# Optimization experiments

Measured on AMD Instinct MI355X. Metric: run time of the kernel, lower is better.

Reference implementation:

```python
import jax, jax.numpy as jnp
import numpy as np

FILTERS = 256
KH, KW = 3, 3
SH, SW = 1, 1
IN_CH = 128


def setup_inputs() -> dict:
    key = jax.random.key(0)
    k1, k2 = jax.random.split(key)
    inputs = jax.random.normal(k1, (32, 112, 112, IN_CH), dtype=jnp.float32)
    # Glorot-uniform init matching the layer's build()
    limit = np.sqrt(6.0 / (KH * KW * IN_CH + FILTERS)).astype(np.float32)
    kernel = jax.random.uniform(k2, (KH, KW, IN_CH, FILTERS), dtype=jnp.float32,
                                minval=-limit, maxval=limit)
    bias = jnp.zeros((FILTERS,), dtype=jnp.float32)
    return {"inputs": inputs, "kernel": kernel, "bias": bias}


def reference(inputs, kernel, bias):
    # Equivalent math to extract_patches(SAME) + flattened matmul + bias:
    # a standard 2D convolution in NHWC with HWIO kernel.
    out = jax.lax.conv_general_dilated(
        inputs, kernel,
        window_strides=(SH, SW),
        padding="SAME",
        dimension_numbers=("NHWC", "HWIO", "NHWC"),
    )
    return out + bias
```

## Files before the change

### kernel.cpp

```cpp
#include <hip/hip_runtime.h>

typedef __attribute__((ext_vector_type(4))) float   floatx4;
typedef __attribute__((ext_vector_type(8))) __bf16  bf16x8;
typedef unsigned short ushort_t;
typedef __attribute__((ext_vector_type(8))) ushort_t ushortx8;

typedef const unsigned int __attribute__((address_space(1)))* gptr_t;
typedef unsigned int __attribute__((address_space(3)))* lptr_t;

#define NIMG 32
#define H    112
#define W    112
#define CIN  128
#define COUT 256
#define HP   114
#define WP   114

#define BM 128
#define BN 128
#define BK 32
#define KSTEPS 36

__device__ __forceinline__ ushort_t f32_to_bf16(float f) {
    unsigned u = __float_as_uint(f);
    unsigned r = 0x7fffu + ((u >> 16) & 1u);
    return (ushort_t)((u + r) >> 16);
}

__global__ __launch_bounds__(256) void prepad_input(const float* __restrict__ in,
                                                    ushort_t* __restrict__ pad) {
    int t   = blockIdx.x * 256 + threadIdx.x;
    int ic8 = t & 15;
    int sp  = t >> 4;
    int iw  = sp % WP;
    int sp2 = sp / WP;
    int ih  = sp2 % HP;
    int n   = sp2 / HP;
    ushortx8 v;
    if (ih >= 1 && ih <= H && iw >= 1 && iw <= W) {
        const float* src = in + ((size_t)((n * H + (ih - 1)) * W + (iw - 1))) * CIN + ic8 * 8;
        floatx4 a = *reinterpret_cast<const floatx4*>(src);
        floatx4 b = *reinterpret_cast<const floatx4*>(src + 4);
#pragma unroll
        for (int j = 0; j < 4; ++j) { v[j] = f32_to_bf16(a[j]); v[4 + j] = f32_to_bf16(b[j]); }
    } else {
#pragma unroll
        for (int j = 0; j < 8; ++j) v[j] = 0;
    }
    reinterpret_cast<ushortx8*>(pad)[t] = v;
}

__global__ __launch_bounds__(256) void wtrans(const float* __restrict__ k,
                                              ushort_t* __restrict__ wt) {
    int t    = blockIdx.x * 256 + threadIdx.x;
    int ic   = t & 127;
    int oc   = (t >> 7) & 255;
    int khkw = t >> 15;
    wt[t] = f32_to_bf16(k[((size_t)(khkw * CIN + ic)) * COUT + oc]);
}

__global__ __launch_bounds__(256) void conv_mfma(const ushort_t* __restrict__ pad,
                                                 const ushort_t* __restrict__ wt,
                                                 const float* __restrict__ bias,
                                                 float* __restrict__ out) {
    __shared__ __align__(16) ushort_t As[BM * BK];
    __shared__ __align__(16) ushort_t Bs[BN * BK];

    const int tid  = threadIdx.x;
    const int wid  = tid >> 6;
    const int lane = tid & 63;
    const int bm   = blockIdx.x >> 1;
    const int bn   = blockIdx.x & 1;

    const int rbase = wid * 32 + (lane >> 2);
    const int kc    = (lane & 3) * 8;

    const ushort_t* aptr[2];
#pragma unroll
    for (int i = 0; i < 2; ++i) {
        int m  = bm * BM + rbase + i * 16;
        int n  = m / (H * W);
        int r  = m % (H * W);
        int oh = r / W;
        int ow = r % W;
        aptr[i] = pad + ((size_t)((n * HP + oh) * WP + ow)) * CIN + kc;
    }
    const ushort_t* bptr[2];
#pragma unroll
    for (int i = 0; i < 2; ++i) {
        int ocr = bn * BN + rbase + i * 16;
        bptr[i] = wt + (size_t)ocr * CIN + kc;
    }
    ushort_t* asd[2];
    ushort_t* bsd[2];
#pragma unroll
    for (int i = 0; i < 2; ++i) {
        asd[i] = As + (wid * 2 + i) * 512;
        bsd[i] = Bs + (wid * 2 + i) * 512;
    }

    const int wr   = wid >> 1, wc = wid & 1;
    const int aoff = (wr * 64 + (lane & 15)) * BK + (lane >> 4) * 8;
    const int boff = (wc * 64 + (lane & 15)) * BK + (lane >> 4) * 8;

    floatx4 acc[4][4];
#pragma unroll
    for (int i = 0; i < 4; ++i)
#pragma unroll
        for (int j = 0; j < 4; ++j) acc[i][j] = (floatx4)0.0f;

    for (int kt = 0; kt < KSTEPS; ++kt) {
        const int kh   = kt / 12;
        const int kw   = (kt >> 2) % 3;
        const int ic0  = (kt & 3) * 32;
        const int offA = (kh * WP + kw) * CIN + ic0;
        const int offB = (kh * 3 + kw) * COUT * CIN + ic0;
#pragma unroll
        for (int i = 0; i < 2; ++i) {
            __builtin_amdgcn_global_load_lds((gptr_t)(aptr[i] + offA), (lptr_t)(asd[i]), 16, 0, 0);
            __builtin_amdgcn_global_load_lds((gptr_t)(bptr[i] + offB), (lptr_t)(bsd[i]), 16, 0, 0);
        }
        __syncthreads();

        bf16x8 af[4], bfr[4];
#pragma unroll
        for (int mi = 0; mi < 4; ++mi)
            af[mi] = *reinterpret_cast<const bf16x8*>(As + aoff + mi * 16 * BK);
#pragma unroll
        for (int ni = 0; ni < 4; ++ni)
            bfr[ni] = *reinterpret_cast<const bf16x8*>(Bs + boff + ni * 16 * BK);
#pragma unroll
        for (int mi = 0; mi < 4; ++mi)
#pragma unroll
            for (int ni = 0; ni < 4; ++ni)
                acc[mi][ni] = __builtin_amdgcn_mfma_f32_16x16x32_bf16(af[mi], bfr[ni], acc[mi][ni], 0, 0, 0);
        __syncthreads();
    }

    const int col0 = bn * BN + wc * 64 + (lane & 15);
    const int row0 = bm * BM + wr * 64 + (lane >> 4) * 4;
#pragma unroll
    for (int ni = 0; ni < 4; ++ni) {
        const float bv = bias[col0 + ni * 16];
#pragma unroll
        for (int mi = 0; mi < 4; ++mi) {
#pragma unroll
            for (int r = 0; r < 4; ++r) {
                out[(size_t)(row0 + mi * 16 + r) * COUT + (col0 + ni * 16)] = acc[mi][ni][r] + bv;
            }
        }
    }
}

extern "C" void kernel_launch(void* const* d_in, const int* in_sizes, int n_in,
                              void* d_out, int out_size, void* d_ws, size_t ws_size,
                              hipStream_t stream) {
    const float* input = (const float*)d_in[0];
    const float* kern  = (const float*)d_in[1];
    const float* bias  = (const float*)d_in[2];
    float* out         = (float*)d_out;

    ushort_t* pad = (ushort_t*)d_ws;
    ushort_t* wt  = pad + (size_t)NIMG * HP * WP * CIN;

    prepad_input<<<25992, 256, 0, stream>>>(input, pad);
    wtrans<<<1152, 256, 0, stream>>>(kern, wt);
    conv_mfma<<<6272, 256, 0, stream>>>(pad, wt, bias, out);
}
```

Baseline: 422.9 us.

## Rewrite implicit-GEMM conv kernel with 256x256 tiles, double-buffered swizzled LDS

Replaces the 128x128x32 single-buffered conv kernel with a 512-thread, 256x256x64 tile kernel that covers all output channels per block. Loads go into double-buffered LDS with an XOR swizzle and are interleaved with MFMA phases, using explicit vmcnt waits, setprio and a block-index remap for L2 locality. The aim is more data reuse per loaded byte, fewer barriers per K step, and overlap of global loads with MFMA work. In exchange it uses 128KB of LDS and many accumulator registers, and the hand-written waitcnt and barrier sequencing is fragile.

Result: faster. 363.8 us (-14.0%).

```diff
diff --git a/kernel.cpp b/kernel.cpp
--- a/kernel.cpp
+++ b/kernel.cpp
@@ -15,11 +15,12 @@
 #define COUT 256
 #define HP   114
 #define WP   114
-
-#define BM 128
-#define BN 128
-#define BK 32
-#define KSTEPS 36
+#define HW   12544
+
+#define BM 256
+#define BN 256
+#define BK 64
+#define NT 18
 
 __device__ __forceinline__ ushort_t f32_to_bf16(float f) {
     unsigned u = __float_as_uint(f);
@@ -59,97 +60,130 @@
     wt[t] = f32_to_bf16(k[((size_t)(khkw * CIN + ic)) * COUT + oc]);
 }
 
-__global__ __launch_bounds__(256) void conv_mfma(const ushort_t* __restrict__ pad,
-                                                 const ushort_t* __restrict__ wt,
-                                                 const float* __restrict__ bias,
-                                                 float* __restrict__ out) {
-    __shared__ __align__(16) ushort_t As[BM * BK];
-    __shared__ __align__(16) ushort_t Bs[BN * BK];
+
+__device__ __forceinline__ int aoffK(int t) {
+    int tap = t >> 1;
+    return ((tap / 3) * WP + (tap % 3)) * CIN + (t & 1) * 64;
+}
+__device__ __forceinline__ int boffK(int t) {
+    int tap = t >> 1;
+    return tap * (COUT * CIN) + (t & 1) * 64;
+}
+
+__global__ __launch_bounds__(512, 2) void conv_mfma8(const ushort_t* __restrict__ pad,
+                                                     const ushort_t* __restrict__ wt,
+                                                     const float* __restrict__ bias,
+                                                     float* __restrict__ out) {
+    __shared__ __align__(16) ushort_t lds[65536];
 
     const int tid  = threadIdx.x;
     const int wid  = tid >> 6;
     const int lane = tid & 63;
-    const int bm   = blockIdx.x >> 1;
-    const int bn   = blockIdx.x & 1;
-
-    const int rbase = wid * 32 + (lane >> 2);
-    const int kc    = (lane & 3) * 8;
-
-    const ushort_t* aptr[2];
-#pragma unroll
-    for (int i = 0; i < 2; ++i) {
-        int m  = bm * BM + rbase + i * 16;
-        int n  = m / (H * W);
-        int r  = m % (H * W);
+    const int wm   = wid >> 2;
+    const int wn   = wid & 3;
+    const int bid  = blockIdx.x;
+    const int bm   = (bid & 7) * 196 + (bid >> 3);
+
+    const int trow = tid >> 3;
+    const int lc   = (tid & 7) ^ (trow & 7);
+
+    const ushort_t* srcA[4];
+    const ushort_t* srcB[4];
+#pragma unroll
+    for (int i = 0; i < 4; ++i) {
+        int m  = bm * BM + i * 64 + trow;
+        int n  = m / HW;
+        int r  = m % HW;
         int oh = r / W;
         int ow = r % W;
-        aptr[i] = pad + ((size_t)((n * HP + oh) * WP + ow)) * CIN + kc;
+        srcA[i] = pad + ((size_t)((n * HP + oh) * WP + ow)) * CIN + lc * 8;
+        int oc = i * 64 + trow;
+        srcB[i] = wt + (size_t)oc * CIN + lc * 8;
     }
-    const ushort_t* bptr[2];
-#pragma unroll
-    for (int i = 0; i < 2; ++i) {
-        int ocr = bn * BN + rbase + i * 16;
-        bptr[i] = wt + (size_t)ocr * CIN + kc;
-    }
-    ushort_t* asd[2];
-    ushort_t* bsd[2];
-#pragma unroll
-    for (int i = 0; i < 2; ++i) {
-        asd[i] = As + (wid * 2 + i) * 512;
-        bsd[i] = Bs + (wid * 2 + i) * 512;
-    }
-
-    const int wr   = wid >> 1, wc = wid & 1;
-    const int aoff = (wr * 64 + (lane & 15)) * BK + (lane >> 4) * 8;
-    const int boff = (wc * 64 + (lane & 15)) * BK + (lane >> 4) * 8;
-
-    floatx4 acc[4][4];
-#pragma unroll
-    for (int i = 0; i < 4; ++i)
+    const int dstSlot = wid * 512;
+
+#define STAGE_A(tile, half)                                                                         \
+    { int _o = aoffK(tile); int _b = ((tile) & 1) * 32768 + (half) * 8192 + dstSlot;                \
+      __builtin_amdgcn_global_load_lds((gptr_t)(srcA[(half)*2+0] + _o), (lptr_t)&lds[_b       ], 16, 0, 0); \
+      __builtin_amdgcn_global_load_lds((gptr_t)(srcA[(half)*2+1] + _o), (lptr_t)&lds[_b + 4096], 16, 0, 0); }
+#define STAGE_B(tile, half)                                                                         \
+    { int _o = boffK(tile); int _b = ((tile) & 1) * 32768 + 16384 + (half) * 8192 + dstSlot;        \
+      __builtin_amdgcn_global_load_lds((gptr_t)(srcB[(half)*2+0] + _o), (lptr_t)&lds[_b       ], 16, 0, 0); \
+      __builtin_amdgcn_global_load_lds((gptr_t)(srcB[(half)*2+1] + _o), (lptr_t)&lds[_b + 4096], 16, 0, 0); }
+
+    const int aBase = wm * 8192 + (lane & 15) * 64;
+    const int bBase = 16384 + (wn >> 1) * 8192 + ((wn & 1) * 64 + (lane & 15)) * 64;
+    int cOff[2];
+#pragma unroll
+    for (int ks = 0; ks < 2; ++ks)
+        cOff[ks] = ((ks * 4 + (lane >> 4)) ^ (lane & 7)) * 8;
+
+    floatx4 acc[8][4];
+#pragma unroll
+    for (int i = 0; i < 8; ++i)
 #pragma unroll
         for (int j = 0; j < 4; ++j) acc[i][j] = (floatx4)0.0f;
 
-    for (int kt = 0; kt < KSTEPS; ++kt) {
-        const int kh   = kt / 12;
-        const int kw   = (kt >> 2) % 3;
-        const int ic0  = (kt & 3) * 32;
-        const int offA = (kh * WP + kw) * CIN + ic0;
-        const int offB = (kh * 3 + kw) * COUT * CIN + ic0;
-#pragma unroll
-        for (int i = 0; i < 2; ++i) {
-            __builtin_amdgcn_global_load_lds((gptr_t)(aptr[i] + offA), (lptr_t)(asd[i]), 16, 0, 0);
-            __builtin_amdgcn_global_load_lds((gptr_t)(bptr[i] + offB), (lptr_t)(bsd[i]), 16, 0, 0);
-        }
-        __syncthreads();
-
-        bf16x8 af[4], bfr[4];
-#pragma unroll
-        for (int mi = 0; mi < 4; ++mi)
-            af[mi] = *reinterpret_cast<const bf16x8*>(As + aoff + mi * 16 * BK);
-#pragma unroll
-        for (int ni = 0; ni < 4; ++ni)
-            bfr[ni] = *reinterpret_cast<const bf16x8*>(Bs + boff + ni * 16 * BK);
-#pragma unroll
-        for (int mi = 0; mi < 4; ++mi)
-#pragma unroll
-            for (int ni = 0; ni < 4; ++ni)
-                acc[mi][ni] = __builtin_amdgcn_mfma_f32_16x16x32_bf16(af[mi], bfr[ni], acc[mi][ni], 0, 0, 0);
-        __syncthreads();
-    }
-
-    const int col0 = bn * BN + wc * 64 + (lane & 15);
-    const int row0 = bm * BM + wr * 64 + (lane >> 4) * 4;
-#pragma unroll
-    for (int ni = 0; ni < 4; ++ni) {
-        const float bv = bias[col0 + ni * 16];
-#pragma unroll
-        for (int mi = 0; mi < 4; ++mi) {
-#pragma unroll
-            for (int r = 0; r < 4; ++r) {
-                out[(size_t)(row0 + mi * 16 + r) * COUT + (col0 + ni * 16)] = acc[mi][ni][r] + bv;
+    STAGE_A(0, 0); STAGE_A(0, 1); STAGE_B(0, 0); STAGE_B(0, 1);
+    STAGE_B(1, 0); STAGE_B(1, 1);
+    asm volatile("s_waitcnt vmcnt(4)" ::: "memory");
+    __builtin_amdgcn_s_barrier();
+
+    for (int t = 0; t < NT; ++t) {
+        const int bufb = (t & 1) * 32768;
+        bf16x8 bfr[4][2];
+#pragma unroll
+        for (int q = 0; q < 4; ++q) {
+            bf16x8 af[2][2];
+#pragma unroll
+            for (int rfl = 0; rfl < 2; ++rfl)
+#pragma unroll
+                for (int ks = 0; ks < 2; ++ks)
+                    af[rfl][ks] = *reinterpret_cast<const bf16x8*>(&lds[bufb + aBase + (2 * q + rfl) * 1024 + cOff[ks]]);
+            if (q == 0) {
+#pragma unroll
+                for (int cf = 0; cf < 4; ++cf)
+#pragma unroll
+                    for (int ks = 0; ks < 2; ++ks)
+                        bfr[cf][ks] = *reinterpret_cast<const bf16x8*>(&lds[bufb + bBase + cf * 1024 + cOff[ks]]);
             }
+            if (q == 0 && t + 1 < NT) STAGE_A(t + 1, 0);
+            if (q == 1 && t + 1 < NT) STAGE_A(t + 1, 1);
+            if (q == 2 && t + 2 < NT) STAGE_B(t + 2, 0);
+            if (q == 3 && t + 2 < NT) STAGE_B(t + 2, 1);
+            __builtin_amdgcn_s_barrier();
+            __builtin_amdgcn_s_setprio(1);
+#pragma unroll
+            for (int rfl = 0; rfl < 2; ++rfl)
+#pragma unroll
+                for (int cf = 0; cf < 4; ++cf)
+#pragma unroll
+                    for (int ks = 0; ks < 2; ++ks)
+                        acc[2 * q + rfl][cf] = __builtin_amdgcn_mfma_f32_16x16x32_bf16(
+                            af[rfl][ks], bfr[cf][ks], acc[2 * q + rfl][cf], 0, 0, 0);
+            __builtin_amdgcn_s_setprio(0);
+            if (q == 3) {
+                if (t < NT - 2)       { asm volatile("s_waitcnt vmcnt(4)" ::: "memory"); }
+                else if (t == NT - 2) { asm volatile("s_waitcnt vmcnt(0)" ::: "memory"); }
+            }
+            __builtin_amdgcn_s_barrier();
         }
     }
+
+    const int col0 = wn * 64 + (lane & 15);
+    const int row0 = bm * BM + wm * 128 + (lane >> 4) * 4;
+    float bv[4];
+#pragma unroll
+    for (int cf = 0; cf < 4; ++cf) bv[cf] = bias[col0 + cf * 16];
+#pragma unroll
+    for (int rf = 0; rf < 8; ++rf)
+#pragma unroll
+        for (int cf = 0; cf < 4; ++cf)
+#pragma unroll
+            for (int r = 0; r < 4; ++r)
+                out[(size_t)(row0 + rf * 16 + r) * COUT + col0 + cf * 16] = acc[rf][cf][r] + bv[cf];
+#undef STAGE_A
+#undef STAGE_B
 }
 
 extern "C" void kernel_launch(void* const* d_in, const int* in_sizes, int n_in,
@@ -165,5 +199,5 @@
 
     prepad_input<<<25992, 256, 0, stream>>>(input, pad);
     wtrans<<<1152, 256, 0, stream>>>(kern, wt);
-    conv_mfma<<<6272, 256, 0, stream>>>(pad, wt, bias, out);
-}
+    conv_mfma8<<<1568, 512, 0, stream>>>(pad, wt, bias, out);
+}
```
